# Performance work log

Measured on AMD Instinct MI355X. Metric: run time of the kernel, lower is better.

Reference implementation:

```python
import jax, jax.numpy as jnp
import numpy as np

DIM = 552          # hidden_dim (divisible by 23 and 24 per outer GroupNorms)
EXPAND = 2
EXP = DIM * EXPAND # expanded_dim = 1104
DS = 16            # d_state
DCONV = 4          # d_conv
SPARSITY = 0.1     # hardcoded sparsity_ratio at block construction
BATCH, SEQ = 8, 4096


def setup_inputs() -> dict:
    key = jax.random.key(0)
    ks = jax.random.split(key, 8)
    s = 0.02
    return {
        "x": jax.random.normal(ks[0], (BATCH, SEQ, DIM), jnp.float32),
        "norm_w": jnp.ones((DIM,), jnp.float32),
        "w_in": jax.random.normal(ks[1], (EXP, DIM), jnp.float32) * s,
        "b_in": jnp.zeros((EXP,), jnp.float32),
        "w_out": jax.random.normal(ks[2], (DIM, EXP), jnp.float32) * s,
        "b_out": jnp.zeros((DIM,), jnp.float32),
        "A": jax.random.normal(ks[3], (DS, DS), jnp.float32) * s,
        "Bp": jax.random.normal(ks[4], (DS,), jnp.float32) * s,
        "Cp": jax.random.normal(ks[5], (EXP, DS), jnp.float32) * s,
        "conv_w": jax.random.normal(ks[6], (EXP, 1, DCONV), jnp.float32) * s,
    }


def _l2norm(v, axis=-1):
    # F.normalize(p=2): v / max(||v||, 1e-12)
    n = jnp.linalg.norm(v, axis=axis, keepdims=True)
    return v / jnp.maximum(n, 1e-12)


def reference(x, norm_w, w_in, b_in, w_out, b_out, A, Bp, Cp, conv_w):
    B, L, C = x.shape
    eps = 1e-6
    # RMSNorm
    rms = jnp.linalg.norm(x, axis=-1, keepdims=True) * (C ** -0.5)
    x_norm = norm_w * (x / (rms + eps))
    x_proj = x_norm @ w_in.T + b_in                              # [B,L,E]
    # similarity routing against the center token
    center = x_proj[:, L // 2]                                   # [B,E]
    sim = jnp.einsum('ble,be->bl', _l2norm(x_proj), _l2norm(center))
    sim = jax.nn.softmax(sim, axis=-1)
    k = max(1, int(L * SPARSITY))
    _, idx = jax.lax.top_k(sim, k)                               # [B,k] descending
    x_sparse = jnp.take_along_axis(x_proj, idx[:, :, None], axis=1)  # [B,k,E]
    # causal depthwise conv over the k selected positions
    xc = jnp.transpose(x_sparse, (0, 2, 1))                      # [B,E,k]
    xc = jax.lax.conv_general_dilated(
        xc, conv_w, (1,), [(DCONV - 1, 0)],
        dimension_numbers=('NCH', 'OIH', 'NCH'),
        feature_group_count=xc.shape[1])
    x_conv = jnp.transpose(xc, (0, 2, 1))                        # [B,k,E]
    # selective SSM recurrence: h = h @ A.T + sigmoid(B)*x_t; y = (h*sigmoid(C)).sum(-1)
    sigB = jax.nn.sigmoid(Bp)                                    # [ds]
    sigC = jax.nn.sigmoid(Cp)                                    # [E,ds]

    def step(h, xt):                                             # h [B,E,ds], xt [B,E]
        h = h @ A.T + sigB * xt[..., None]
        return h, jnp.einsum('bes,es->be', h, sigC)

    h0 = jnp.zeros((B, x_conv.shape[-1], A.shape[0]), x.dtype)
    _, outs = jax.lax.scan(step, h0, jnp.transpose(x_conv, (1, 0, 2)))  # [k,B,E]
    x_proc = jnp.transpose(outs, (1, 0, 2)) @ w_out.T + b_out   # [B,k,C]
    # scatter back to the full sequence (topk indices are unique -> set)
    out = jnp.zeros_like(x).at[jnp.arange(B)[:, None], idx].set(x_proc)
    return out + x
```

## Files before the change

### kernel.cpp

```cpp
#include <hip/hip_runtime.h>
#include <hip/hip_bf16.h>

#define BB 8
#define LL 4096
#define CC 552
#define EE 1104
#define KT 409
#define M1 32768
#define M2 3272
#define KP 576
#define KP2 1120
#define M2P 3328
#define JT 16
#define JC 19
#define NQT 5
#define GKC 224

typedef __attribute__((ext_vector_type(8))) short bf16x8;
typedef __attribute__((ext_vector_type(4))) float f32x4;

__device__ __forceinline__ ushort f2bf(float f) {
    unsigned u = __float_as_uint(f);
    return (ushort)((u + 0x7FFFu + ((u >> 16) & 1u)) >> 16);
}
__device__ __forceinline__ float bf2f(ushort h) {
    return __uint_as_float(((unsigned)h) << 16);
}

__device__ __forceinline__ void gl_lds16(const ushort* g, ushort* l) {
    __builtin_amdgcn_global_load_lds(
        (const __attribute__((address_space(1))) void*)g,
        (__attribute__((address_space(3))) void*)l, 16, 0, 0);
}

__global__ void prep_kernel(const float* __restrict__ w_in, const float* __restrict__ norm_w,
                            float* __restrict__ winp, float* __restrict__ winpT,
                            float* __restrict__ qpart, int* __restrict__ posm) {
    int i = blockIdx.x * blockDim.x + threadIdx.x;
    if (i < NQT * M1) qpart[i] = 0.f;
    if (i < M1) posm[i] = -1;
    if (i < EE * CC) {
        int c = i % CC, e = i / CC;
        float v = w_in[i] * norm_w[c];
        winp[i] = v;
        winpT[(size_t)c * EE + e] = v;
    }
}

__global__ __launch_bounds__(256) void convx_kernel(const float* __restrict__ x,
                                                    const double* __restrict__ gbuf,
                                                    ushort* __restrict__ xh, ushort* __restrict__ xl,
                                                    float* __restrict__ inv,
                                                    double* __restrict__ dval) {
    const int wave = threadIdx.x >> 6, lane = threadIdx.x & 63;
    const int r = blockIdx.x * 4 + wave;
    const int b = r >> 12;
    const float* xr = x + (size_t)r * CC;
    const double* gb = gbuf + (size_t)b * CC;
    ushort* oh = xh + (size_t)r * KP;
    ushort* ol = xl + (size_t)r * KP;
    float ss = 0.f;
    double d = 0.0;
#pragma unroll
    for (int k = 0; k < 3; k++) {
        const int c = lane + k * 64;
        if (c < 144) {
            float4 v = make_float4(0.f, 0.f, 0.f, 0.f);
            if (c < 138) {
                v = reinterpret_cast<const float4*>(xr)[c];
                ss += v.x * v.x + v.y * v.y + v.z * v.z + v.w * v.w;
                const double* gp = gb + c * 4;
                d += (double)v.x * gp[0] + (double)v.y * gp[1] +
                     (double)v.z * gp[2] + (double)v.w * gp[3];
            }
            ushort4 h, l;
            h.x = f2bf(v.x); l.x = f2bf(v.x - bf2f(h.x));
            h.y = f2bf(v.y); l.y = f2bf(v.y - bf2f(h.y));
            h.z = f2bf(v.z); l.z = f2bf(v.z - bf2f(h.z));
            h.w = f2bf(v.w); l.w = f2bf(v.w - bf2f(h.w));
            reinterpret_cast<ushort4*>(oh)[c] = h;
            reinterpret_cast<ushort4*>(ol)[c] = l;
        }
    }
#pragma unroll
    for (int o = 32; o > 0; o >>= 1) { ss += __shfl_down(ss, o, 64); d += __shfl_down(d, o, 64); }
    if (lane == 0) {
        inv[r] = 1.f / (sqrtf(ss / (float)CC) + 1e-6f);
        dval[r] = d;
    }
}

__device__ __forceinline__ void conv_row_kp_hi(const float* __restrict__ src, int n, int nvalid,
                                               ushort* __restrict__ wh, int t) {
    if (t >= 144) return;
    float4 v = make_float4(0.f, 0.f, 0.f, 0.f);
    if (n < nvalid && t < 138) v = reinterpret_cast<const float4*>(src + (size_t)n * CC)[t];
    ushort4 h;
    h.x = f2bf(v.x); h.y = f2bf(v.y); h.z = f2bf(v.z); h.w = f2bf(v.w);
    reinterpret_cast<ushort4*>(wh + (size_t)n * KP)[t] = h;
}

__device__ __forceinline__ void conv_row_kp2_hi(const float* __restrict__ src, int n,
                                                ushort* __restrict__ wh, int t) {
    for (int i = t; i < KP2 / 4; i += 256) {
        float4 v = make_float4(0.f, 0.f, 0.f, 0.f);
        if (n < CC && i < EE / 4) v = reinterpret_cast<const float4*>(src + (size_t)n * EE)[i];
        ushort4 h;
        h.x = f2bf(v.x); h.y = f2bf(v.y); h.z = f2bf(v.z); h.w = f2bf(v.w);
        reinterpret_cast<ushort4*>(wh + (size_t)n * KP2)[i] = h;
    }
}

__device__ __forceinline__ void conv_row_kp2_full(const float* __restrict__ src, int n,
                                                  ushort* __restrict__ wh, ushort* __restrict__ wl, int t) {
    for (int i = t; i < KP2 / 4; i += 256) {
        float4 v = make_float4(0.f, 0.f, 0.f, 0.f);
        if (n < CC && i < EE / 4) v = reinterpret_cast<const float4*>(src + (size_t)n * EE)[i];
        ushort4 h, l;
        h.x = f2bf(v.x); l.x = f2bf(v.x - bf2f(h.x));
        h.y = f2bf(v.y); l.y = f2bf(v.y - bf2f(h.y));
        h.z = f2bf(v.z); l.z = f2bf(v.z - bf2f(h.z));
        h.w = f2bf(v.w); l.w = f2bf(v.w - bf2f(h.w));
        reinterpret_cast<ushort4*>(wh + (size_t)n * KP2)[i] = h;
        reinterpret_cast<ushort4*>(wl + (size_t)n * KP2)[i] = l;
    }
}

__device__ void taps19_body(const float* __restrict__ A, const float* __restrict__ Bp,
                            const float* __restrict__ Cp, const float* __restrict__ conv_w,
                            float* __restrict__ ck19, int t) {
    __shared__ float Ash[256];
    __shared__ float vmat[JT][16];
    Ash[t] = A[t];
    __syncthreads();
    if (t < 16) vmat[0][t] = 1.f / (1.f + expf(-Bp[t]));
    __syncthreads();
    for (int j = 1; j < JT; j++) {
        float nv = 0.f;
        if (t < 16) {
#pragma unroll
            for (int s2 = 0; s2 < 16; s2++) nv += Ash[t * 16 + s2] * vmat[j - 1][s2];
        }
        __syncthreads();
        if (t < 16) vmat[j][t] = nv;
        __syncthreads();
    }
    for (int e = t; e < EE; e += 256) {
        float sc[16];
#pragma unroll
        for (int s = 0; s < 16; s++) sc[s] = 1.f / (1.f + expf(-Cp[e * 16 + s]));
        float ck[JT];
#pragma unroll
        for (int j = 0; j < JT; j++) {
            float kk = 0.f;
#pragma unroll
            for (int s = 0; s < 16; s++) kk += sc[s] * vmat[j][s];
            ck[j] = kk;
        }
        float w4[4];
#pragma unroll
        for (int i = 0; i < 4; i++) w4[i] = conv_w[e * 4 + 3 - i];
#pragma unroll
        for (int m = 0; m < JC; m++) {
            float kk = 0.f;
#pragma unroll
            for (int i = 0; i < 4; i++) {
                int jm = m - i;
                if (jm >= 0 && jm < JT) kk += w4[i] * ck[jm];
            }
            ck19[m * EE + e] = kk;
        }
    }
}

__global__ __launch_bounds__(256) void wconv_fused(
    const float* __restrict__ winp, const float* __restrict__ w_out,
    const float* __restrict__ winpT,
    const float* __restrict__ A, const float* __restrict__ Bp,
    const float* __restrict__ Cp, const float* __restrict__ conv_w,
    ushort* __restrict__ wh,
    ushort* __restrict__ w2h,
    ushort* __restrict__ wth, ushort* __restrict__ wtl,
    float* __restrict__ ck19) {
    int bx = blockIdx.x;
    const int t = threadIdx.x;
    if (bx < 1152) { conv_row_kp_hi(winp, bx, EE, wh, t); return; }
    bx -= 1152;
    if (bx < 640) { conv_row_kp2_hi(w_out, bx, w2h, t); return; }
    bx -= 640;
    if (bx < 640) { conv_row_kp2_full(winpT, bx, wth, wtl, t); return; }
    taps19_body(A, Bp, Cp, conv_w, ck19, t);
}

__global__ __launch_bounds__(256) void convG_kernel(const float* __restrict__ Gp,
                                                    ushort* __restrict__ gh, ushort* __restrict__ gl) {
    const int n = blockIdx.x, t = threadIdx.x;
    if (t >= 144) return;
    float4 v = make_float4(0.f, 0.f, 0.f, 0.f);
    if (n < CC && t < 138) {
#pragma unroll
        for (int c = 0; c < 5; c++) {
            float4 p = reinterpret_cast<const float4*>(Gp + (size_t)c * 640 * CC + (size_t)n * CC)[t];
            v = make_float4(v.x + p.x, v.y + p.y, v.z + p.z, v.w + p.w);
        }
        const int k0 = t * 4;
        float m0 = (n > k0 + 0) ? 2.f : (n == k0 + 0) ? 1.f : 0.f;
        float m1 = (n > k0 + 1) ? 2.f : (n == k0 + 1) ? 1.f : 0.f;
        float m2 = (n > k0 + 2) ? 2.f : (n == k0 + 2) ? 1.f : 0.f;
        float m3 = (n > k0 + 3) ? 2.f : (n == k0 + 3) ? 1.f : 0.f;
        v = make_float4(v.x * m0, v.y * m1, v.z * m2, v.w * m3);
    }
    ushort4 h, l;
    h.x = f2bf(v.x); l.x = f2bf(v.x - bf2f(h.x));
    h.y = f2bf(v.y); l.y = f2bf(v.y - bf2f(h.y));
    h.z = f2bf(v.z); l.z = f2bf(v.z - bf2f(h.z));
    h.w = f2bf(v.w); l.w = f2bf(v.w - bf2f(h.w));
    reinterpret_cast<ushort4*>(gh + (size_t)n * KP)[t] = h;
    reinterpret_cast<ushort4*>(gl + (size_t)n * KP)[t] = l;
}

__global__ __launch_bounds__(256) void gemmG_kernel(
    const ushort* __restrict__ Wh, const ushort* __restrict__ Wl,
    float* __restrict__ Gp) {
    __shared__ ushort As_h[2][128][32];
    __shared__ ushort As_l[2][128][32];
    __shared__ ushort Bs_h[2][128][32];
    __shared__ ushort Bs_l[2][128][32];
    const int tid = threadIdx.x;
    const int col0 = blockIdx.x * 128;
    const int row0 = blockIdx.y * 128;
    const int kbeg = blockIdx.z * GKC;
    const int kend = kbeg + GKC;
    const int wave = tid >> 6, lane = tid & 63;
    const int wr = (wave >> 1) * 64, wc = (wave & 1) * 64;
    const int lrow = lane & 15, kb = (lane >> 4) * 8;

    const int s0 = wave * 32 + (lane >> 2);
    const int skh = (lane & 3) * 8;
    const ushort* gAh0 = Wh + (size_t)(row0 + s0) * KP2 + skh;
    const ushort* gAl0 = Wl + (size_t)(row0 + s0) * KP2 + skh;
    const ushort* gBh0 = Wh + (size_t)(col0 + s0) * KP2 + skh;
    const ushort* gBl0 = Wl + (size_t)(col0 + s0) * KP2 + skh;
    const size_t rstep = (size_t)16 * KP2;

    f32x4 acc[4][4];
    const f32x4 zero = {0.f, 0.f, 0.f, 0.f};
#pragma unroll
    for (int i = 0; i < 4; i++)
#pragma unroll
        for (int j = 0; j < 4; j++) acc[i][j] = zero;

    auto stage = [&](int buf, int k0) {
        gl_lds16(gAh0 + k0, &As_h[buf][wave * 32][0]);
        gl_lds16(gAh0 + rstep + k0, &As_h[buf][wave * 32 + 16][0]);
        gl_lds16(gAl0 + k0, &As_l[buf][wave * 32][0]);
        gl_lds16(gAl0 + rstep + k0, &As_l[buf][wave * 32 + 16][0]);
        gl_lds16(gBh0 + k0, &Bs_h[buf][wave * 32][0]);
        gl_lds16(gBh0 + rstep + k0, &Bs_h[buf][wave * 32 + 16][0]);
        gl_lds16(gBl0 + k0, &Bs_l[buf][wave * 32][0]);
        gl_lds16(gBl0 + rstep + k0, &Bs_l[buf][wave * 32 + 16][0]);
    };
    auto compute = [&](int buf) {
        bf16x8 ah[4], al[4], bh[4], bl[4];
#pragma unroll
        for (int i = 0; i < 4; i++) {
            ah[i] = *reinterpret_cast<const bf16x8*>(&As_h[buf][wr + i * 16 + lrow][kb]);
            al[i] = *reinterpret_cast<const bf16x8*>(&As_l[buf][wr + i * 16 + lrow][kb]);
            bh[i] = *reinterpret_cast<const bf16x8*>(&Bs_h[buf][wc + i * 16 + lrow][kb]);
            bl[i] = *reinterpret_cast<const bf16x8*>(&Bs_l[buf][wc + i * 16 + lrow][kb]);
        }
#pragma unroll
        for (int i = 0; i < 4; i++)
#pragma unroll
            for (int j = 0; j < 4; j++) {
                acc[i][j] = __builtin_amdgcn_mfma_f32_16x16x32_bf16(ah[i], bh[j], acc[i][j], 0, 0, 0);
                acc[i][j] = __builtin_amdgcn_mfma_f32_16x16x32_bf16(ah[i], bl[j], acc[i][j], 0, 0, 0);
                acc[i][j] = __builtin_amdgcn_mfma_f32_16x16x32_bf16(al[i], bh[j], acc[i][j], 0, 0, 0);
            }
    };

    stage(0, kbeg);
    __syncthreads();
    int cur = 0;
    for (int k0 = kbeg + 32; k0 < kend; k0 += 32) {
        stage(cur ^ 1, k0);
        compute(cur);
        __syncthreads();
        cur ^= 1;
    }
    compute(cur);

    float* Gc = Gp + (size_t)blockIdx.z * 640 * CC;
#pragma unroll
    for (int i = 0; i < 4; i++) {
        const int gmb = row0 + wr + i * 16 + (lane >> 4) * 4;
#pragma unroll
        for (int reg = 0; reg < 4; reg++) {
            const int gm = gmb + reg;
            if (gm < CC) {
#pragma unroll
                for (int j = 0; j < 4; j++) {
                    const int gn = col0 + wc + j * 16 + lrow;
                    if (gn < CC) Gc[(size_t)gm * CC + gn] = acc[i][j][reg];
                }
            }
        }
    }
}

__global__ __launch_bounds__(256) void gemm_mfma_1x(
    const ushort* __restrict__ Ah,
    const ushort* __restrict__ Bh,
    const float* __restrict__ rowscale, const float* __restrict__ bias,
    float* __restrict__ C, int ldc, int M, int N, int Kp, int r0) {
    __shared__ ushort As[2][128][32];
    __shared__ ushort Bs[2][128][32];
    const int tid = threadIdx.x;
    const int col0 = blockIdx.x * 128;
    const int row0 = blockIdx.y * 128;
    const int wave = tid >> 6, lane = tid & 63;
    const int wr = (wave >> 1) * 64, wc = (wave & 1) * 64;
    const int lrow = lane & 15, kb = (lane >> 4) * 8;

    const int s0 = wave * 32 + (lane >> 2);
    const int skh = (lane & 3) * 8;
    const ushort* gA0 = Ah + (size_t)(row0 + s0) * Kp + skh;
    const ushort* gB0 = Bh + (size_t)(col0 + s0) * Kp + skh;
    const size_t rstep = (size_t)16 * Kp;

    f32x4 acc[4][4];
    const f32x4 zero = {0.f, 0.f, 0.f, 0.f};
#pragma unroll
    for (int i = 0; i < 4; i++)
#pragma unroll
        for (int j = 0; j < 4; j++) acc[i][j] = zero;

    auto stage = [&](int buf, int k0) {
        gl_lds16(gA0 + k0, &As[buf][wave * 32][0]);
        gl_lds16(gA0 + rstep + k0, &As[buf][wave * 32 + 16][0]);
        gl_lds16(gB0 + k0, &Bs[buf][wave * 32][0]);
        gl_lds16(gB0 + rstep + k0, &Bs[buf][wave * 32 + 16][0]);
    };
    auto compute = [&](int buf) {
        bf16x8 ah[4], bh[4];
#pragma unroll
        for (int i = 0; i < 4; i++) {
            ah[i] = *reinterpret_cast<const bf16x8*>(&As[buf][wr + i * 16 + lrow][kb]);
            bh[i] = *reinterpret_cast<const bf16x8*>(&Bs[buf][wc + i * 16 + lrow][kb]);
        }
#pragma unroll
        for (int i = 0; i < 4; i++)
#pragma unroll
            for (int j = 0; j < 4; j++)
                acc[i][j] = __builtin_amdgcn_mfma_f32_16x16x32_bf16(ah[i], bh[j], acc[i][j], 0, 0, 0);
    };

    stage(0, 0);
    __syncthreads();
    int cur = 0;
    for (int k0 = 32; k0 < Kp; k0 += 32) {
        stage(cur ^ 1, k0);
        compute(cur);
        __syncthreads();
        cur ^= 1;
    }
    compute(cur);

#pragma unroll
    for (int i = 0; i < 4; i++) {
        const int gmb = r0 + row0 + wr + i * 16 + (lane >> 4) * 4;
#pragma unroll
        for (int reg = 0; reg < 4; reg++) {
            const int gm = gmb + reg;
            if (gm < M) {
                const float rs = rowscale ? rowscale[gm] : 1.f;
#pragma unroll
                for (int j = 0; j < 4; j++) {
                    const int gn = col0 + wc + j * 16 + lrow;
                    if (gn < N) C[(size_t)gm * ldc + gn] = acc[i][j][reg] * rs + (bias ? bias[gn] : 0.f);
                }
            }
        }
    }
}

__global__ __launch_bounds__(256) void gemm_mfma_q(
    const ushort* __restrict__ Ah, const ushort* __restrict__ Al,
    const ushort* __restrict__ Bh, const ushort* __restrict__ Bl,
    float* __restrict__ qpart) {
    __shared__ ushort As_h[128][32];
    __shared__ ushort As_l[128][32];
    __shared__ ushort Bs_h[128][32];
    __shared__ ushort Bs_l[128][32];
    const int tid = threadIdx.x;
    const int orig = blockIdx.x;
    const int work = (orig & 7) * 160 + (orig >> 3);
    const int ct = work % NQT;
    const int rt = work / NQT;
    const int col0 = ct * 128;
    const int row0 = rt * 128;
    const int kend = (KP < col0 + 128) ? KP : (col0 + 128);
    const int wave = tid >> 6, lane = tid & 63;
    const int wr = (wave >> 1) * 64, wc = (wave & 1) * 64;
    const int lrow = lane & 15, kb = (lane >> 4) * 8;

    const int s0 = wave * 32 + (lane >> 2);
    const int skh = (lane & 3) * 8;
    const ushort* gAh0 = Ah + (size_t)(row0 + s0) * KP + skh;
    const ushort* gAl0 = Al + (size_t)(row0 + s0) * KP + skh;
    const ushort* gBh0 = Bh + (size_t)(col0 + s0) * KP + skh;
    const ushort* gBl0 = Bl + (size_t)(col0 + s0) * KP + skh;
    const size_t rstep = (size_t)16 * KP;
    ushort* lAh0 = &As_h[wave * 32][0];      ushort* lAh1 = &As_h[wave * 32 + 16][0];
    ushort* lAl0 = &As_l[wave * 32][0];      ushort* lAl1 = &As_l[wave * 32 + 16][0];
    ushort* lBh0 = &Bs_h[wave * 32][0];      ushort* lBh1 = &Bs_h[wave * 32 + 16][0];
    ushort* lBl0 = &Bs_l[wave * 32][0];      ushort* lBl1 = &Bs_l[wave * 32 + 16][0];

    f32x4 acc[4][4];
    const f32x4 zero = {0.f, 0.f, 0.f, 0.f};
#pragma unroll
    for (int i = 0; i < 4; i++)
#pragma unroll
        for (int j = 0; j < 4; j++) acc[i][j] = zero;

    for (int k0 = 0; k0 < kend; k0 += 32) {
        __syncthreads();
        gl_lds16(gAh0 + k0, lAh0); gl_lds16(gAh0 + rstep + k0, lAh1);
        gl_lds16(gAl0 + k0, lAl0); gl_lds16(gAl0 + rstep + k0, lAl1);
        gl_lds16(gBh0 + k0, lBh0); gl_lds16(gBh0 + rstep + k0, lBh1);
        gl_lds16(gBl0 + k0, lBl0); gl_lds16(gBl0 + rstep + k0, lBl1);
        __syncthreads();
        bf16x8 ah[4], al[4], bh[4], bl[4];
#pragma unroll
        for (int i = 0; i < 4; i++) {
            ah[i] = *reinterpret_cast<const bf16x8*>(&As_h[wr + i * 16 + lrow][kb]);
            al[i] = *reinterpret_cast<const bf16x8*>(&As_l[wr + i * 16 + lrow][kb]);
            bh[i] = *reinterpret_cast<const bf16x8*>(&Bs_h[wc + i * 16 + lrow][kb]);
            bl[i] = *reinterpret_cast<const bf16x8*>(&Bs_l[wc + i * 16 + lrow][kb]);
        }
#pragma unroll
        for (int i = 0; i < 4; i++)
#pragma unroll
            for (int j = 0; j < 4; j++) {
                acc[i][j] = __builtin_amdgcn_mfma_f32_16x16x32_bf16(ah[i], bh[j], acc[i][j], 0, 0, 0);
                acc[i][j] = __builtin_amdgcn_mfma_f32_16x16x32_bf16(ah[i], bl[j], acc[i][j], 0, 0, 0);
                acc[i][j] = __builtin_amdgcn_mfma_f32_16x16x32_bf16(al[i], bh[j], acc[i][j], 0, 0, 0);
            }
    }

    float* qp = qpart + (size_t)ct * M1;
#pragma unroll
    for (int i = 0; i < 4; i++) {
#pragma unroll
        for (int reg = 0; reg < 4; reg++) {
            const int gm = row0 + wr + i * 16 + (lane >> 4) * 4 + reg;
            float part = 0.f;
#pragma unroll
            for (int j = 0; j < 4; j++) {
                const int gn = col0 + wc + j * 16 + lrow;
                float xv = 0.f;
                if (gn < CC) {
                    const size_t o = (size_t)gm * KP + gn;
                    xv = bf2f(Ah[o]) + bf2f(Al[o]);
                }
                part += acc[i][j][reg] * xv;
            }
#pragma unroll
            for (int o = 1; o < 16; o <<= 1) part += __shfl_xor(part, o, 64);
            if ((lane & 15) == 0) atomicAdd(&qp[gm], part);
        }
    }
}

__global__ __launch_bounds__(256) void center_kernel(const float* __restrict__ x,
                                                     double* __restrict__ xcn) {
    __shared__ double red[4];
    const int b = blockIdx.x, tid = threadIdx.x;
    const float* xc = x + ((size_t)(b * LL + LL / 2)) * CC;
    double s = 0.0;
    for (int c = tid; c < CC; c += 256) { double v = xc[c]; s += v * v; }
#pragma unroll
    for (int o = 32; o > 0; o >>= 1) s += __shfl_down(s, o, 64);
    if ((tid & 63) == 0) red[tid >> 6] = s;
    __syncthreads();
    const double tot = red[0] + red[1] + red[2] + red[3];
    const double invc = 1.0 / (sqrt(tot / (double)CC) + 1e-6);
    for (int c = tid; c < CC; c += 256) xcn[(size_t)b * CC + c] = (double)xc[c] * invc;
}

__global__ __launch_bounds__(256) void gram1_kernel(const float* __restrict__ winp,
                                                    const double* __restrict__ xcn,
                                                    double* __restrict__ t1) {
    const int b = blockIdx.y;
    const int wave = threadIdx.x >> 6, lane = threadIdx.x & 63;
    const int e = blockIdx.x * 4 + wave;
    const float* wr = winp + (size_t)e * CC;
    const double* xb = xcn + (size_t)b * CC;
    double s = 0.0;
    for (int c = lane; c < CC; c += 64) s += (double)wr[c] * xb[c];
#pragma unroll
    for (int o = 32; o > 0; o >>= 1) s += __shfl_down(s, o, 64);
    if (lane == 0) t1[(size_t)b * EE + e] = s;
}

__global__ __launch_bounds__(256) void gram2_kernel(const float* __restrict__ winpT,
                                                    const double* __restrict__ t1,
                                                    double* __restrict__ g) {
    const int b = blockIdx.y;
    const int wave = threadIdx.x >> 6, lane = threadIdx.x & 63;
    const int c = blockIdx.x * 4 + wave;
    if (c >= CC) return;
    const float* wr = winpT + (size_t)c * EE;
    const double* tb = t1 + (size_t)b * EE;
    double s = 0.0;
    for (int e = lane; e < EE; e += 64) s += (double)wr[e] * tb[e];
#pragma unroll
    for (int o = 32; o > 0; o >>= 1) s += __shfl_down(s, o, 64);
    if (lane == 0) g[(size_t)b * CC + c] = s;
}

__global__ __launch_bounds__(1024) void topk_kernel(const double* __restrict__ dval,
                                                    const float* __restrict__ qpart,
                                                    int* __restrict__ idx) {
    __shared__ unsigned long long keys[4096];
    const int b = blockIdx.x;
    for (int i = threadIdx.x; i < 4096; i += 1024) {
        const int r = b * 4096 + i;
        double q = 0.0;
#pragma unroll
        for (int t5 = 0; t5 < NQT; t5++) q += (double)qpart[(size_t)t5 * M1 + r];
        const float sv = (float)(dval[r] / sqrt(fmax(q, 1e-30)));
        unsigned u = __float_as_uint(sv);
        u = (u & 0x80000000u) ? ~u : (u | 0x80000000u);
        keys[i] = ((unsigned long long)(~u) << 32) | (unsigned)i;
    }
    __syncthreads();
    for (int size = 2; size <= 4096; size <<= 1) {
        for (int stride = size >> 1; stride > 0; stride >>= 1) {
#pragma unroll 1
            for (int t = threadIdx.x; t < 2048; t += 1024) {
                int low = t & (stride - 1);
                int pos = ((t - low) << 1) + low;
                bool up = ((pos & size) == 0);
                unsigned long long ka = keys[pos], kb = keys[pos + stride];
                if ((ka > kb) == up) { keys[pos] = kb; keys[pos + stride] = ka; }
            }
            __syncthreads();
        }
    }
    for (int t = threadIdx.x; t < KT; t += 1024) idx[b * KT + t] = (int)(keys[t] & 0xffffffffu);
}

__global__ __launch_bounds__(256) void gatherx_kernel(const ushort* __restrict__ xh,
                                                      const float* __restrict__ inv,
                                                      const int* __restrict__ idx,
                                                      ushort* __restrict__ sh,
                                                      float* __restrict__ invsel,
                                                      int* __restrict__ pos) {
    const int r = blockIdx.x, t = threadIdx.x;
    if (r >= M2) {
        if (t < 144) reinterpret_cast<ushort4*>(sh + (size_t)r * KP)[t] = make_ushort4(0, 0, 0, 0);
        return;
    }
    const int b = r / KT;
    const int src = b * LL + idx[r];
    if (t < 144) {
        reinterpret_cast<ushort4*>(sh + (size_t)r * KP)[t] =
            reinterpret_cast<const ushort4*>(xh + (size_t)src * KP)[t];
    }
    if (t == 0) {
        invsel[r] = inv[src];
        pos[src] = r;
    }
}

__global__ __launch_bounds__(256) void conv19_kernel(const float* __restrict__ xps,
                                                     const float* __restrict__ ck19,
                                                     ushort* __restrict__ oh) {
    const int r = blockIdx.x, t = threadIdx.x;
    ushort* ph = oh + (size_t)r * KP2;
    if (r >= M2) {
        for (int e = t; e < KP2; e += 256) ph[e] = 0;
        return;
    }
    const int b = r / KT, tt = r - b * KT;
    const int jmax = (tt < JC - 1) ? tt : (JC - 1);
    const float* base = xps + (size_t)r * EE;
    for (int e = t; e < KP2; e += 256) {
        float y = 0.f;
        if (e < EE) {
            const float* bp = base + e;
            for (int j = 0; j <= jmax; j++) y += ck19[j * EE + e] * bp[-(ptrdiff_t)j * EE];
        }
        ph[e] = f2bf(y);
    }
}

__global__ __launch_bounds__(256) void outfuse_kernel(const float* __restrict__ x,
                                                      const float* __restrict__ xproc,
                                                      const int* __restrict__ pos,
                                                      float* __restrict__ out) {
    const int wave = threadIdx.x >> 6, lane = threadIdx.x & 63;
    const int r = blockIdx.x * 4 + wave;
    const int p = pos[r];
    const float4* xr = reinterpret_cast<const float4*>(x + (size_t)r * CC);
    float4* orow = reinterpret_cast<float4*>(out + (size_t)r * CC);
    const float4* pr = (p >= 0) ? reinterpret_cast<const float4*>(xproc + (size_t)p * CC) : nullptr;
#pragma unroll
    for (int k = 0; k < 3; k++) {
        const int c = lane + k * 64;
        if (c < 138) {
            float4 v = xr[c];
            if (pr) {
                float4 a = pr[c];
                v = make_float4(v.x + a.x, v.y + a.y, v.z + a.z, v.w + a.w);
            }
            orow[c] = v;
        }
    }
}

extern "C" void kernel_launch(void* const* d_in, const int* in_sizes, int n_in,
                              void* d_out, int out_size, void* d_ws, size_t ws_size,
                              hipStream_t stream) {
    const float* x      = (const float*)d_in[0];
    const float* norm_w = (const float*)d_in[1];
    const float* w_in   = (const float*)d_in[2];
    const float* b_in   = (const float*)d_in[3];
    const float* w_out  = (const float*)d_in[4];
    const float* b_out  = (const float*)d_in[5];
    const float* Amat   = (const float*)d_in[6];
    const float* Bp     = (const float*)d_in[7];
    const float* Cp     = (const float*)d_in[8];
    const float* conv_w = (const float*)d_in[9];
    float* out = (float*)d_out;

    char* wsb = (char*)d_ws;
    size_t off = 0;
    auto take = [&](size_t bytes) {
        void* p = wsb + off;
        off += (bytes + 255) & ~(size_t)255;
        return p;
    };
    ushort* xh    = (ushort*)take((size_t)M1 * KP * 2);
    ushort* xl    = (ushort*)take((size_t)M1 * KP * 2);
    float*  winp  = (float*)take((size_t)EE * CC * 4);
    float*  winpT = (float*)take((size_t)EE * CC * 4);
    ushort* wh    = (ushort*)take((size_t)1152 * KP * 2);
    ushort* w2h   = (ushort*)take((size_t)640 * KP2 * 2);
    ushort* wth   = (ushort*)take((size_t)640 * KP2 * 2);
    ushort* wtl   = (ushort*)take((size_t)640 * KP2 * 2);
    float*  Gp    = (float*)take((size_t)5 * 640 * CC * 4);
    ushort* Gh    = (ushort*)take((size_t)640 * KP * 2);
    ushort* Gl    = (ushort*)take((size_t)640 * KP * 2);
    float*  inv   = (float*)take((size_t)M1 * 4);
    float*  qpart = (float*)take((size_t)NQT * M1 * 4);
    double* dval  = (double*)take((size_t)M1 * 8);
    int*    posm  = (int*)take((size_t)M1 * 4);
    int*    idxb  = (int*)take((size_t)BB * KT * 4);
    double* gbuf  = (double*)take((size_t)BB * CC * 8);
    double* xcn   = (double*)take((size_t)BB * CC * 8);
    double* t1b   = (double*)take((size_t)BB * EE * 8);
    float*  ck19  = (float*)take((size_t)JC * EE * 4);
    ushort* sh    = (ushort*)take((size_t)M2P * KP * 2);
    float*  invsel= (float*)take((size_t)M2P * 4);
    float*  xps   = (float*)take((size_t)M2P * EE * 4);
    ushort* o2h   = (ushort*)take((size_t)M2P * KP2 * 2);
    float*  xproc = (float*)take((size_t)M2P * CC * 4);
    (void)ws_size;

    prep_kernel<<<(EE * CC + 255) / 256, 256, 0, stream>>>(w_in, norm_w, winp, winpT, qpart, posm);

    center_kernel<<<BB, 256, 0, stream>>>(x, xcn);
    dim3 gg1(EE / 4, BB);
    gram1_kernel<<<gg1, 256, 0, stream>>>(winp, xcn, t1b);
    dim3 gg2(CC / 4, BB);
    gram2_kernel<<<gg2, 256, 0, stream>>>(winpT, t1b, gbuf);

    wconv_fused<<<1152 + 640 + 640 + 1, 256, 0, stream>>>(
        winp, w_out, winpT, Amat, Bp, Cp, conv_w, wh, w2h, wth, wtl, ck19);

    convx_kernel<<<M1 / 4, 256, 0, stream>>>(x, gbuf, xh, xl, inv, dval);

    dim3 gG(5, 5, 5);
    gemmG_kernel<<<gG, 256, 0, stream>>>(wth, wtl, Gp);
    convG_kernel<<<640, 256, 0, stream>>>(Gp, Gh, Gl);

    gemm_mfma_q<<<NQT * (M1 / 128), 256, 0, stream>>>(xh, xl, Gh, Gl, qpart);

    topk_kernel<<<BB, 1024, 0, stream>>>(dval, qpart, idxb);

    gatherx_kernel<<<M2P, 256, 0, stream>>>(xh, inv, idxb, sh, invsel, posm);
    dim3 g1(9, M2P / 128);
    gemm_mfma_1x<<<g1, 256, 0, stream>>>(sh, wh, invsel, b_in, xps,
                                         EE, M2, EE, KP, 0);

    conv19_kernel<<<M2P, 256, 0, stream>>>(xps, ck19, o2h);

    dim3 g3(5, M2P / 128);
    gemm_mfma_1x<<<g3, 256, 0, stream>>>(o2h, w2h, nullptr, b_out, xproc,
                                         CC, M2, CC, KP2, 0);

    outfuse_kernel<<<M1 / 4, 256, 0, stream>>>(x, xproc, posm, out);
}
```

Baseline: 365.8 us.

## Fuse gather into GEMM, merge center/prep kernels, use 64x64 GEMM tiles

Drops the separate gatherx kernel: the first projection GEMM now reads the selected rows of xh directly through topk indices and applies the per-row inverse norm in its epilogue, while topk writes the position map. The center-norm kernel is folded into prep as extra blocks, and the q GEMM reads x in fp32 for its dot product instead of rebuilding it from hi/lo bf16. Both small GEMMs switch from 128x128 double-buffered tiles to 64x64 single-buffered tiles to get more blocks on the small M2 problem. The cost is less data reuse per tile and no overlap between loads and MFMA compute.

Result: faster. 320.7 us (-12.3%).

```diff
diff --git a/kernel.cpp b/kernel.cpp
--- a/kernel.cpp
+++ b/kernel.cpp
@@ -15,6 +15,7 @@
 #define JC 19
 #define NQT 5
 #define GKC 224
+#define NCB ((EE * CC + 255) / 256)
 
 typedef __attribute__((ext_vector_type(8))) short bf16x8;
 typedef __attribute__((ext_vector_type(4))) float f32x4;
@@ -33,18 +34,37 @@
         (__attribute__((address_space(3))) void*)l, 16, 0, 0);
 }
 
-__global__ void prep_kernel(const float* __restrict__ w_in, const float* __restrict__ norm_w,
-                            float* __restrict__ winp, float* __restrict__ winpT,
-                            float* __restrict__ qpart, int* __restrict__ posm) {
-    int i = blockIdx.x * blockDim.x + threadIdx.x;
-    if (i < NQT * M1) qpart[i] = 0.f;
-    if (i < M1) posm[i] = -1;
-    if (i < EE * CC) {
-        int c = i % CC, e = i / CC;
-        float v = w_in[i] * norm_w[c];
-        winp[i] = v;
-        winpT[(size_t)c * EE + e] = v;
-    }
+__global__ __launch_bounds__(256) void prep_kernel(const float* __restrict__ w_in,
+                                                   const float* __restrict__ norm_w,
+                                                   const float* __restrict__ x,
+                                                   float* __restrict__ winp, float* __restrict__ winpT,
+                                                   float* __restrict__ qpart, int* __restrict__ posm,
+                                                   double* __restrict__ xcn) {
+    const int bx = blockIdx.x;
+    if (bx < NCB) {
+        int i = bx * 256 + threadIdx.x;
+        if (i < NQT * M1) qpart[i] = 0.f;
+        if (i < M1) posm[i] = -1;
+        if (i < EE * CC) {
+            int c = i % CC, e = i / CC;
+            float v = w_in[i] * norm_w[c];
+            winp[i] = v;
+            winpT[(size_t)c * EE + e] = v;
+        }
+        return;
+    }
+    __shared__ double red[4];
+    const int b = bx - NCB, tid = threadIdx.x;
+    const float* xc = x + ((size_t)(b * LL + LL / 2)) * CC;
+    double s = 0.0;
+    for (int c = tid; c < CC; c += 256) { double v = xc[c]; s += v * v; }
+#pragma unroll
+    for (int o = 32; o > 0; o >>= 1) s += __shfl_down(s, o, 64);
+    if ((tid & 63) == 0) red[tid >> 6] = s;
+    __syncthreads();
+    const double tot = red[0] + red[1] + red[2] + red[3];
+    const double invc = 1.0 / (sqrt(tot / (double)CC) + 1e-6);
+    for (int c = tid; c < CC; c += 256) xcn[(size_t)b * CC + c] = (double)xc[c] * invc;
 }
 
 __global__ __launch_bounds__(256) void convx_kernel(const float* __restrict__ x,
@@ -308,76 +328,59 @@
     }
 }
 
-__global__ __launch_bounds__(256) void gemm_mfma_1x(
+__global__ __launch_bounds__(256) void gemm64(
     const ushort* __restrict__ Ah,
+    const int* __restrict__ idxb,
+    const float* __restrict__ inv,
     const ushort* __restrict__ Bh,
-    const float* __restrict__ rowscale, const float* __restrict__ bias,
-    float* __restrict__ C, int ldc, int M, int N, int Kp, int r0) {
-    __shared__ ushort As[2][128][32];
-    __shared__ ushort Bs[2][128][32];
-    const int tid = threadIdx.x;
-    const int col0 = blockIdx.x * 128;
-    const int row0 = blockIdx.y * 128;
-    const int wave = tid >> 6, lane = tid & 63;
-    const int wr = (wave >> 1) * 64, wc = (wave & 1) * 64;
+    const float* __restrict__ bias,
+    float* __restrict__ C, int ldc, int M, int Nmask, int Kp) {
+    __shared__ ushort As[64][32];
+    __shared__ ushort Bs[64][32];
+    const int tid = threadIdx.x, wave = tid >> 6, lane = tid & 63;
+    const int col0 = blockIdx.x * 64, row0 = blockIdx.y * 64;
     const int lrow = lane & 15, kb = (lane >> 4) * 8;
-
-    const int s0 = wave * 32 + (lane >> 2);
-    const int skh = (lane & 3) * 8;
-    const ushort* gA0 = Ah + (size_t)(row0 + s0) * Kp + skh;
-    const ushort* gB0 = Bh + (size_t)(col0 + s0) * Kp + skh;
-    const size_t rstep = (size_t)16 * Kp;
-
-    f32x4 acc[4][4];
+    const int wr = (wave >> 1) * 32, wc = (wave & 1) * 32;
+
+    const int sar = row0 + wave * 16 + (lane >> 2);
+    int asrc = sar;
+    if (idxb) asrc = (sar < M) ? (sar / KT) * LL + idxb[sar] : 0;
+    const ushort* gA = Ah + (size_t)asrc * Kp + (lane & 3) * 8;
+    const ushort* gB = Bh + (size_t)(col0 + wave * 16 + (lane >> 2)) * Kp + (lane & 3) * 8;
+    ushort* lA = &As[wave * 16][0];
+    ushort* lB = &Bs[wave * 16][0];
+
+    f32x4 acc[2][2];
     const f32x4 zero = {0.f, 0.f, 0.f, 0.f};
-#pragma unroll
-    for (int i = 0; i < 4; i++)
-#pragma unroll
-        for (int j = 0; j < 4; j++) acc[i][j] = zero;
-
-    auto stage = [&](int buf, int k0) {
-        gl_lds16(gA0 + k0, &As[buf][wave * 32][0]);
-        gl_lds16(gA0 + rstep + k0, &As[buf][wave * 32 + 16][0]);
-        gl_lds16(gB0 + k0, &Bs[buf][wave * 32][0]);
-        gl_lds16(gB0 + rstep + k0, &Bs[buf][wave * 32 + 16][0]);
-    };
-    auto compute = [&](int buf) {
-        bf16x8 ah[4], bh[4];
-#pragma unroll
-        for (int i = 0; i < 4; i++) {
-            ah[i] = *reinterpret_cast<const bf16x8*>(&As[buf][wr + i * 16 + lrow][kb]);
-            bh[i] = *reinterpret_cast<const bf16x8*>(&Bs[buf][wc + i * 16 + lrow][kb]);
-        }
-#pragma unroll
-        for (int i = 0; i < 4; i++)
-#pragma unroll
-            for (int j = 0; j < 4; j++)
-                acc[i][j] = __builtin_amdgcn_mfma_f32_16x16x32_bf16(ah[i], bh[j], acc[i][j], 0, 0, 0);
-    };
-
-    stage(0, 0);
-    __syncthreads();
-    int cur = 0;
-    for (int k0 = 32; k0 < Kp; k0 += 32) {
-        stage(cur ^ 1, k0);
-        compute(cur);
+    acc[0][0] = zero; acc[0][1] = zero; acc[1][0] = zero; acc[1][1] = zero;
+
+    for (int k0 = 0; k0 < Kp; k0 += 32) {
         __syncthreads();
-        cur ^= 1;
-    }
-    compute(cur);
-
-#pragma unroll
-    for (int i = 0; i < 4; i++) {
-        const int gmb = r0 + row0 + wr + i * 16 + (lane >> 4) * 4;
+        gl_lds16(gA + k0, lA);
+        gl_lds16(gB + k0, lB);
+        __syncthreads();
+        bf16x8 a0 = *reinterpret_cast<const bf16x8*>(&As[wr + lrow][kb]);
+        bf16x8 a1 = *reinterpret_cast<const bf16x8*>(&As[wr + 16 + lrow][kb]);
+        bf16x8 b0 = *reinterpret_cast<const bf16x8*>(&Bs[wc + lrow][kb]);
+        bf16x8 b1 = *reinterpret_cast<const bf16x8*>(&Bs[wc + 16 + lrow][kb]);
+        acc[0][0] = __builtin_amdgcn_mfma_f32_16x16x32_bf16(a0, b0, acc[0][0], 0, 0, 0);
+        acc[0][1] = __builtin_amdgcn_mfma_f32_16x16x32_bf16(a0, b1, acc[0][1], 0, 0, 0);
+        acc[1][0] = __builtin_amdgcn_mfma_f32_16x16x32_bf16(a1, b0, acc[1][0], 0, 0, 0);
+        acc[1][1] = __builtin_amdgcn_mfma_f32_16x16x32_bf16(a1, b1, acc[1][1], 0, 0, 0);
+    }
+
+#pragma unroll
+    for (int i = 0; i < 2; i++) {
 #pragma unroll
         for (int reg = 0; reg < 4; reg++) {
-            const int gm = gmb + reg;
+            const int gm = row0 + wr + i * 16 + (lane >> 4) * 4 + reg;
             if (gm < M) {
-                const float rs = rowscale ? rowscale[gm] : 1.f;
-#pragma unroll
-                for (int j = 0; j < 4; j++) {
+                float rs = 1.f;
+                if (idxb && inv) rs = inv[(gm / KT) * LL + idxb[gm]];
+#pragma unroll
+                for (int j = 0; j < 2; j++) {
                     const int gn = col0 + wc + j * 16 + lrow;
-                    if (gn < N) C[(size_t)gm * ldc + gn] = acc[i][j][reg] * rs + (bias ? bias[gn] : 0.f);
+                    if (gn < Nmask) C[(size_t)gm * ldc + gn] = acc[i][j][reg] * rs + bias[gn];
                 }
             }
         }
@@ -387,7 +390,7 @@
 __global__ __launch_bounds__(256) void gemm_mfma_q(
     const ushort* __restrict__ Ah, const ushort* __restrict__ Al,
     const ushort* __restrict__ Bh, const ushort* __restrict__ Bl,
-    float* __restrict__ qpart) {
+    const float* __restrict__ xsrc, float* __restrict__ qpart) {
     __shared__ ushort As_h[128][32];
     __shared__ ushort As_l[128][32];
     __shared__ ushort Bs_h[128][32];
@@ -458,11 +461,7 @@
 #pragma unroll
             for (int j = 0; j < 4; j++) {
                 const int gn = col0 + wc + j * 16 + lrow;
-                float xv = 0.f;
-                if (gn < CC) {
-                    const size_t o = (size_t)gm * KP + gn;
-                    xv = bf2f(Ah[o]) + bf2f(Al[o]);
-                }
+                const float xv = (gn < CC) ? xsrc[(size_t)gm * CC + gn] : 0.f;
                 part += acc[i][j][reg] * xv;
             }
 #pragma unroll
@@ -470,22 +469,6 @@
             if ((lane & 15) == 0) atomicAdd(&qp[gm], part);
         }
     }
-}
-
-__global__ __launch_bounds__(256) void center_kernel(const float* __restrict__ x,
-                                                     double* __restrict__ xcn) {
-    __shared__ double red[4];
-    const int b = blockIdx.x, tid = threadIdx.x;
-    const float* xc = x + ((size_t)(b * LL + LL / 2)) * CC;
-    double s = 0.0;
-    for (int c = tid; c < CC; c += 256) { double v = xc[c]; s += v * v; }
-#pragma unroll
-    for (int o = 32; o > 0; o >>= 1) s += __shfl_down(s, o, 64);
-    if ((tid & 63) == 0) red[tid >> 6] = s;
-    __syncthreads();
-    const double tot = red[0] + red[1] + red[2] + red[3];
-    const double invc = 1.0 / (sqrt(tot / (double)CC) + 1e-6);
-    for (int c = tid; c < CC; c += 256) xcn[(size_t)b * CC + c] = (double)xc[c] * invc;
 }
 
 __global__ __launch_bounds__(256) void gram1_kernel(const float* __restrict__ winp,
@@ -521,7 +504,8 @@
 
 __global__ __launch_bounds__(1024) void topk_kernel(const double* __restrict__ dval,
                                                     const float* __restrict__ qpart,
-                                                    int* __restrict__ idx) {
+                                                    int* __restrict__ idx,
+                                                    int* __restrict__ pos) {
     __shared__ unsigned long long keys[4096];
     const int b = blockIdx.x;
     for (int i = threadIdx.x; i < 4096; i += 1024) {
@@ -540,37 +524,18 @@
 #pragma unroll 1
             for (int t = threadIdx.x; t < 2048; t += 1024) {
                 int low = t & (stride - 1);
-                int pos = ((t - low) << 1) + low;
-                bool up = ((pos & size) == 0);
-                unsigned long long ka = keys[pos], kb = keys[pos + stride];
-                if ((ka > kb) == up) { keys[pos] = kb; keys[pos + stride] = ka; }
+                int p2 = ((t - low) << 1) + low;
+                bool up = ((p2 & size) == 0);
+                unsigned long long ka = keys[p2], kb2 = keys[p2 + stride];
+                if ((ka > kb2) == up) { keys[p2] = kb2; keys[p2 + stride] = ka; }
             }
             __syncthreads();
         }
     }
-    for (int t = threadIdx.x; t < KT; t += 1024) idx[b * KT + t] = (int)(keys[t] & 0xffffffffu);
-}
-
-__global__ __launch_bounds__(256) void gatherx_kernel(const ushort* __restrict__ xh,
-                                                      const float* __restrict__ inv,
-                                                      const int* __restrict__ idx,
-                                                      ushort* __restrict__ sh,
-                                                      float* __restrict__ invsel,
-                                                      int* __restrict__ pos) {
-    const int r = blockIdx.x, t = threadIdx.x;
-    if (r >= M2) {
-        if (t < 144) reinterpret_cast<ushort4*>(sh + (size_t)r * KP)[t] = make_ushort4(0, 0, 0, 0);
-        return;
-    }
-    const int b = r / KT;
-    const int src = b * LL + idx[r];
-    if (t < 144) {
-        reinterpret_cast<ushort4*>(sh + (size_t)r * KP)[t] =
-            reinterpret_cast<const ushort4*>(xh + (size_t)src * KP)[t];
-    }
-    if (t == 0) {
-        invsel[r] = inv[src];
-        pos[src] = r;
+    for (int t = threadIdx.x; t < KT; t += 1024) {
+        const int iv = (int)(keys[t] & 0xffffffffu);
+        idx[b * KT + t] = iv;
+        pos[b * LL + iv] = b * KT + t;
     }
 }
 
@@ -662,16 +627,13 @@
     double* xcn   = (double*)take((size_t)BB * CC * 8);
     double* t1b   = (double*)take((size_t)BB * EE * 8);
     float*  ck19  = (float*)take((size_t)JC * EE * 4);
-    ushort* sh    = (ushort*)take((size_t)M2P * KP * 2);
-    float*  invsel= (float*)take((size_t)M2P * 4);
     float*  xps   = (float*)take((size_t)M2P * EE * 4);
     ushort* o2h   = (ushort*)take((size_t)M2P * KP2 * 2);
     float*  xproc = (float*)take((size_t)M2P * CC * 4);
     (void)ws_size;
 
-    prep_kernel<<<(EE * CC + 255) / 256, 256, 0, stream>>>(w_in, norm_w, winp, winpT, qpart, posm);
-
-    center_kernel<<<BB, 256, 0, stream>>>(x, xcn);
+    prep_kernel<<<NCB + BB, 256, 0, stream>>>(w_in, norm_w, x, winp, winpT, qpart, posm, xcn);
+
     dim3 gg1(EE / 4, BB);
     gram1_kernel<<<gg1, 256, 0, stream>>>(winp, xcn, t1b);
     dim3 gg2(CC / 4, BB);
@@ -686,20 +648,17 @@
     gemmG_kernel<<<gG, 256, 0, stream>>>(wth, wtl, Gp);
     convG_kernel<<<640, 256, 0, stream>>>(Gp, Gh, Gl);
 
-    gemm_mfma_q<<<NQT * (M1 / 128), 256, 0, stream>>>(xh, xl, Gh, Gl, qpart);
-
-    topk_kernel<<<BB, 1024, 0, stream>>>(dval, qpart, idxb);
-
-    gatherx_kernel<<<M2P, 256, 0, stream>>>(xh, inv, idxb, sh, invsel, posm);
-    dim3 g1(9, M2P / 128);
-    gemm_mfma_1x<<<g1, 256, 0, stream>>>(sh, wh, invsel, b_in, xps,
-                                         EE, M2, EE, KP, 0);
+    gemm_mfma_q<<<NQT * (M1 / 128), 256, 0, stream>>>(xh, xl, Gh, Gl, x, qpart);
+
+    topk_kernel<<<BB, 1024, 0, stream>>>(dval, qpart, idxb, posm);
+
+    dim3 g1(1152 / 64, M2P / 64);
+    gemm64<<<g1, 256, 0, stream>>>(xh, idxb, inv, wh, b_in, xps, EE, M2, EE, KP);
 
     conv19_kernel<<<M2P, 256, 0, stream>>>(xps, ck19, o2h);
 
-    dim3 g3(5, M2P / 128);
-    gemm_mfma_1x<<<g3, 256, 0, stream>>>(o2h, w2h, nullptr, b_out, xproc,
-                                         CC, M2, CC, KP2, 0);
+    dim3 g3(640 / 64, M2P / 64);
+    gemm64<<<g3, 256, 0, stream>>>(o2h, nullptr, nullptr, w2h, b_out, xproc, CC, M2, CC, KP2);
 
     outfuse_kernel<<<M1 / 4, 256, 0, stream>>>(x, xproc, posm, out);
 }
```
